# Kernel optimization log

Hardware: AMD Instinct MI355X
Metric: run time of the kernel (lower is better)

## Reference

```python
import jax, jax.numpy as jnp
import numpy as np

L, B, N, D, K = 32, 4, 1000, 128, 8


def setup_inputs() -> dict:
    key = jax.random.key(0)
    ks = jax.random.split(key, 10)
    w = lambda k, s: (jax.random.normal(k, s, jnp.float32) * 0.05)
    return {
        "x": jax.random.normal(ks[0], (L, B, N, D), jnp.float32),
        "route_neighbors": jax.random.randint(ks[1], (N, K), 0, N),
        "t_in_w": w(ks[2], (3 * D, D)),
        "t_in_b": w(ks[3], (3 * D,)),
        "t_out_w": w(ks[4], (D, D)),
        "t_out_b": w(ks[5], (D,)),
        "s_in_w": w(ks[6], (3 * D, D)),
        "s_in_b": w(ks[7], (3 * D,)),
        "s_out_w": w(ks[8], (D, D)),
        "s_out_b": w(ks[9], (D,)),
        "n_heads": 8,
    }


def reference(x, route_neighbors, t_in_w, t_in_b, t_out_w, t_out_b,
              s_in_w, s_in_b, s_out_w, s_out_b, n_heads):
    l, b, n, d = x.shape
    h = n_heads
    dh = d // h
    scale = 1.0 / jnp.sqrt(jnp.asarray(dh, x.dtype))

    # ---- temporal MHA: attend over time axis L, batch = (B, N) ----
    wq, wk, wv = jnp.split(t_in_w, 3, axis=0)
    bq, bk, bv = jnp.split(t_in_b, 3, axis=0)
    q = (x @ wq.T + bq).reshape(l, b, n, h, dh)
    k = (x @ wk.T + bk).reshape(l, b, n, h, dh)
    v = (x @ wv.T + bv).reshape(l, b, n, h, dh)
    scores = jnp.einsum('lbnhd,mbnhd->bnhlm', q, k) * scale
    attn = jax.nn.softmax(scores, axis=-1)
    o = jnp.einsum('bnhlm,mbnhd->lbnhd', attn, v).reshape(l, b, n, d)
    t_out = o @ t_out_w.T + t_out_b

    # ---- spatial MHA: per node, single-token query over K gathered neighbors ----
    swq, swk, swv = jnp.split(s_in_w, 3, axis=0)
    sbq, sbk, sbv = jnp.split(s_in_b, 3, axis=0)
    xn = x[:, :, route_neighbors]                         # (L,B,N,K,D) gather
    sq = (x @ swq.T + sbq).reshape(l, b, n, h, dh)
    sk = (xn @ swk.T + sbk).reshape(l, b, n, -1, h, dh)
    sv = (xn @ swv.T + sbv).reshape(l, b, n, -1, h, dh)
    s_scores = jnp.einsum('lbnhd,lbnkhd->lbnhk', sq, sk) * scale
    s_attn = jax.nn.softmax(s_scores, axis=-1)
    so = jnp.einsum('lbnhk,lbnkhd->lbnhd', s_attn, sv).reshape(l, b, n, d)
    s_out = so @ s_out_w.T + s_out_b

    return t_out + s_out
```

## Files before the change

kernel.cpp:

```cpp
#include <hip/hip_runtime.h>
#include <math.h>

#define L_ 32
#define B_ 4
#define N_ 1000
#define D_ 128
#define H_ 8
#define DH_ 16
#define KN_ 8
#define M_ (L_ * B_ * N_)

typedef __attribute__((ext_vector_type(8))) short short8;
typedef __attribute__((ext_vector_type(8))) unsigned short ushort8v;
typedef __attribute__((ext_vector_type(4))) float floatx4;
typedef __attribute__((ext_vector_type(4))) unsigned uintx4;

static __device__ __forceinline__ unsigned short f2bf(float f) {
  union { float f; unsigned u; } v; v.f = f;
  unsigned r = v.u + 0x7fffu + ((v.u >> 16) & 1u);
  return (unsigned short)(r >> 16);
}
static __device__ __forceinline__ float bf2f(unsigned short s) {
  union { unsigned u; float f; } v; v.u = ((unsigned)s) << 16;
  return v.f;
}
static __device__ __forceinline__ unsigned cvtpk(float lo, float hi) {
  unsigned r;
  asm("v_cvt_pk_bf16_f32 %0, %1, %2" : "=v"(r) : "v"(lo), "v"(hi));
  return r;
}
static __device__ __forceinline__ float vexp2(float x) {
  float r; asm("v_exp_f32 %0, %1" : "=v"(r) : "v"(x)); return r;
}
static __device__ __forceinline__ float vrcp(float x) {
  float r; asm("v_rcp_f32 %0, %1" : "=v"(r) : "v"(x)); return r;
}
union B8 { uintx4 u; short8 s; };
static __device__ __forceinline__ void gload_lds16(const unsigned short* g,
                                                   unsigned short* l) {
  __builtin_amdgcn_global_load_lds(
      (const __attribute__((address_space(1))) unsigned int*)g,
      (__attribute__((address_space(3))) unsigned int*)l, 16, 0, 0);
}

__global__ __launch_bounds__(256) void prep_kernel(
    const float* __restrict__ x, const float* __restrict__ wt_in,
    const float* __restrict__ ws_in, const float* __restrict__ wt_out,
    const float* __restrict__ ws_out, unsigned short* __restrict__ ximg,
    unsigned short* __restrict__ wimg) {
  const int bid = blockIdx.x, t = threadIdx.x;
  const float* src;
  unsigned short* dst;
  if (bid < 1000) {
    src = x + (size_t)bid * 16384;
    dst = ximg + (size_t)bid * 16384;
  } else {
    int w = bid - 1000;
    if (w < 3) src = wt_in + (size_t)w * 16384;
    else if (w < 6) src = ws_in + (size_t)(w - 3) * 16384;
    else if (w == 6) src = wt_out;
    else src = ws_out;
    dst = wimg + (size_t)w * 16384;
  }
#pragma unroll
  for (int it = 0; it < 8; ++it) {
    int gi = it * 256 + t;
    int m = gi >> 4, g = gi & 15;
    const float4* sp = (const float4*)(src + m * 128 + g * 8);
    float4 a = sp[0], b = sp[1];
    ushort8v o;
    o[0] = f2bf(a.x); o[1] = f2bf(a.y); o[2] = f2bf(a.z); o[3] = f2bf(a.w);
    o[4] = f2bf(b.x); o[5] = f2bf(b.y); o[6] = f2bf(b.z); o[7] = f2bf(b.w);
    *(ushort8v*)(dst + (size_t)(m * 16 + (g ^ (m & 7))) * 8) = o;
  }
}

__global__ __launch_bounds__(256) void proj_mfma(
    const unsigned short* __restrict__ ximg,
    const unsigned short* __restrict__ wimg, const float* __restrict__ bias,
    unsigned short* __restrict__ out) {
  __shared__ unsigned short As[128 * 128];
  __shared__ unsigned short Bs[128 * 128];
  const int t = threadIdx.x;
  const int bm = blockIdx.x / 3, bn = blockIdx.x % 3;
  const unsigned short* aSrc = ximg + (size_t)bm * 16384;
  const unsigned short* bSrc = wimg + (size_t)bn * 16384;
#pragma unroll
  for (int it = 0; it < 8; ++it) {
    int gi = it * 256 + t;
    gload_lds16(aSrc + (size_t)gi * 8, &As[gi * 8]);
    gload_lds16(bSrc + (size_t)gi * 8, &Bs[gi * 8]);
  }
  __syncthreads();
  const int wave = t >> 6, lane = t & 63;
  const int wm = (wave >> 1) * 64, wn = (wave & 1) * 64;
  const int lq = lane >> 4, l16 = lane & 15;
  floatx4 acc[4][4] = {};
#pragma unroll
  for (int kk = 0; kk < 4; ++kk) {
    int g = kk * 4 + lq;
    short8 a[4], b[4];
#pragma unroll
    for (int i = 0; i < 4; ++i) {
      int ma = wm + i * 16 + l16;
      a[i] = *(const short8*)(&As[(ma * 16 + (g ^ (ma & 7))) * 8]);
      int nb = wn + i * 16 + l16;
      b[i] = *(const short8*)(&Bs[(nb * 16 + (g ^ (nb & 7))) * 8]);
    }
#pragma unroll
    for (int i = 0; i < 4; ++i)
#pragma unroll
      for (int j = 0; j < 4; ++j)
        acc[i][j] = __builtin_amdgcn_mfma_f32_16x16x32_bf16(a[i], b[j],
                                                            acc[i][j], 0, 0, 0);
  }
  const size_t rowBase = (size_t)bm * 128 + wm;
  const int colBase = bn * 128 + wn;
#pragma unroll
  for (int j = 0; j < 4; ++j) {
    float bb = bias[colBase + j * 16 + l16];
#pragma unroll
    for (int i = 0; i < 4; ++i) {
#pragma unroll
      for (int r = 0; r < 4; ++r) {
        size_t row = rowBase + i * 16 + lq * 4 + r;
        out[row * 384 + colBase + j * 16 + l16] = f2bf(acc[i][j][r] + bb);
      }
    }
  }
}

__global__ __launch_bounds__(256) void tattn_fused(
    const unsigned short* __restrict__ ximg,
    const unsigned short* __restrict__ wimg,
    const float* __restrict__ bias,
    unsigned short* __restrict__ oimg) {
  __shared__ unsigned short Sx[512 * 8];
  __shared__ unsigned short Sqk[4][2][32 * 40];
  const int t = threadIdx.x;
  const int b = blockIdx.x / N_;
  const int n = blockIdx.x % N_;
  const int c = b * N_ + n;
#pragma unroll
  for (int it = 0; it < 2; ++it) {
    const int s = it * 256 + t;
    const int ml = s >> 4, gs = s & 15;
    const int G = gs ^ (ml & 7);
    const size_t rg = (size_t)ml * (B_ * N_) + c;
    gload_lds16(ximg + (rg >> 7) * 16384 +
                    ((rg & 127) * 16 + (size_t)(G ^ ((int)rg & 7))) * 8,
                &Sx[s * 8]);
  }
  asm volatile("s_waitcnt vmcnt(0)" ::: "memory");
  __syncthreads();

  const int wv = t >> 6, lane = t & 63;
  const int lq = lane >> 4, l16 = lane & 15;

  floatx4 aQ[2][2] = {}, aK[2][2] = {}, aV[2][2] = {};
#pragma unroll
  for (int kk = 0; kk < 4; ++kk) {
    short8 a[2];
#pragma unroll
    for (int i = 0; i < 2; ++i) {
      const int ml = i * 16 + l16;
      a[i] = *(const short8*)&Sx[(ml * 16 + ((kk * 4 + lq) ^ (ml & 7))) * 8];
    }
#pragma unroll
    for (int mat = 0; mat < 3; ++mat) {
      const unsigned short* wb = wimg + mat * 16384;
      short8 bf[2];
#pragma unroll
      for (int j = 0; j < 2; ++j) {
        const int nb = wv * 32 + j * 16 + l16;
        bf[j] =
            *(const short8*)&wb[(nb * 16 + ((kk * 4 + lq) ^ (nb & 7))) * 8];
      }
#pragma unroll
      for (int i = 0; i < 2; ++i)
#pragma unroll
        for (int j = 0; j < 2; ++j) {
          floatx4* acc = mat == 0 ? &aQ[i][j] : (mat == 1 ? &aK[i][j] : &aV[i][j]);
          *acc = __builtin_amdgcn_mfma_f32_16x16x32_bf16(a[i], bf[j], *acc, 0,
                                                         0, 0);
        }
    }
  }
  const float bQ0 = bias[wv * 32 + l16], bQ1 = bias[wv * 32 + 16 + l16];
  const float bK0 = bias[128 + wv * 32 + l16],
              bK1 = bias[128 + wv * 32 + 16 + l16];
  const float bV0 = bias[256 + wv * 32 + l16],
              bV1 = bias[256 + wv * 32 + 16 + l16];
  unsigned short* Sq = Sqk[wv][0];
  unsigned short* Sk = Sqk[wv][1];
#pragma unroll
  for (int i = 0; i < 2; ++i)
#pragma unroll
    for (int j = 0; j < 2; ++j) {
      const float qb_ = j ? bQ1 : bQ0, kb_ = j ? bK1 : bK0;
      const unsigned q01 = cvtpk(aQ[i][j][0] + qb_, aQ[i][j][1] + qb_);
      const unsigned q23 = cvtpk(aQ[i][j][2] + qb_, aQ[i][j][3] + qb_);
      const unsigned k01 = cvtpk(aK[i][j][0] + kb_, aK[i][j][1] + kb_);
      const unsigned k23 = cvtpk(aK[i][j][2] + kb_, aK[i][j][3] + kb_);
      unsigned short* q_ = &Sq[(i * 16 + lq * 4) * 40 + j * 16 + l16];
      unsigned short* k_ = &Sk[(i * 16 + lq * 4) * 40 + j * 16 + l16];
      q_[0] = (unsigned short)q01;   q_[40] = (unsigned short)(q01 >> 16);
      q_[80] = (unsigned short)q23;  q_[120] = (unsigned short)(q23 >> 16);
      k_[0] = (unsigned short)k01;   k_[40] = (unsigned short)(k01 >> 16);
      k_[80] = (unsigned short)k23;  k_[120] = (unsigned short)(k23 >> 16);
    }
  unsigned short* ob[8];
  int rsw[8];
#pragma unroll
  for (int lt = 0; lt < 2; ++lt)
#pragma unroll
    for (int r = 0; r < 4; ++r) {
      const int l = lt * 16 + lq * 4 + r;
      const size_t rg = (size_t)l * (B_ * N_) + c;
      ob[lt * 4 + r] = oimg + (rg >> 7) * 16384 + (size_t)(rg & 127) * 128;
      rsw[lt * 4 + r] = (int)(rg & 7);
    }

  const float CSC = 0.25f * 1.4426950408889634f;
#pragma unroll
  for (int hh = 0; hh < 2; ++hh) {
    const int h = wv * 2 + hh;
    short8 ka0 = {}, ka1 = {}, qb0 = {}, qb1 = {};
    if (lq < 2) {
      const int go = (2 * hh + lq) * 8;
      ka0 = *(const short8*)&Sk[l16 * 40 + go];
      ka1 = *(const short8*)&Sk[(16 + l16) * 40 + go];
      qb0 = *(const short8*)&Sq[l16 * 40 + go];
      qb1 = *(const short8*)&Sq[(16 + l16) * 40 + go];
    }
    floatx4 st00 = {}, st01 = {}, st10 = {}, st11 = {};
    st00 = __builtin_amdgcn_mfma_f32_16x16x32_bf16(ka0, qb0, st00, 0, 0, 0);
    st01 = __builtin_amdgcn_mfma_f32_16x16x32_bf16(ka0, qb1, st01, 0, 0, 0);
    st10 = __builtin_amdgcn_mfma_f32_16x16x32_bf16(ka1, qb0, st10, 0, 0, 0);
    st11 = __builtin_amdgcn_mfma_f32_16x16x32_bf16(ka1, qb1, st11, 0, 0, 0);
    const float bV = hh ? bV1 : bV0;
    B8 vu;
    vu.u[0] = cvtpk(aV[0][hh][0] + bV, aV[0][hh][1] + bV);
    vu.u[1] = cvtpk(aV[0][hh][2] + bV, aV[0][hh][3] + bV);
    vu.u[2] = cvtpk(aV[1][hh][0] + bV, aV[1][hh][1] + bV);
    vu.u[3] = cvtpk(aV[1][hh][2] + bV, aV[1][hh][3] + bV);
    const short8 vb = vu.s;
    short8 pa0, pa1;
    {
      floatx4 a = st00 * CSC, cc = st10 * CSC;
      float mx = fmaxf(fmaxf(fmaxf(a[0], a[1]), fmaxf(a[2], a[3])),
                       fmaxf(fmaxf(cc[0], cc[1]), fmaxf(cc[2], cc[3])));
      mx = fmaxf(mx, __shfl_xor(mx, 16));
      mx = fmaxf(mx, __shfl_xor(mx, 32));
      float p0 = vexp2(a[0] - mx), p1 = vexp2(a[1] - mx);
      float p2 = vexp2(a[2] - mx), p3 = vexp2(a[3] - mx);
      float p4 = vexp2(cc[0] - mx), p5 = vexp2(cc[1] - mx);
      float p6 = vexp2(cc[2] - mx), p7 = vexp2(cc[3] - mx);
      float sm = ((p0 + p1) + (p2 + p3)) + ((p4 + p5) + (p6 + p7));
      sm += __shfl_xor(sm, 16);
      sm += __shfl_xor(sm, 32);
      const float inv = vrcp(sm);
      B8 pu;
      pu.u[0] = cvtpk(p0 * inv, p1 * inv);
      pu.u[1] = cvtpk(p2 * inv, p3 * inv);
      pu.u[2] = cvtpk(p4 * inv, p5 * inv);
      pu.u[3] = cvtpk(p6 * inv, p7 * inv);
      pa0 = pu.s;
    }
    {
      floatx4 a = st01 * CSC, cc = st11 * CSC;
      float mx = fmaxf(fmaxf(fmaxf(a[0], a[1]), fmaxf(a[2], a[3])),
                       fmaxf(fmaxf(cc[0], cc[1]), fmaxf(cc[2], cc[3])));
      mx = fmaxf(mx, __shfl_xor(mx, 16));
      mx = fmaxf(mx, __shfl_xor(mx, 32));
      float p0 = vexp2(a[0] - mx), p1 = vexp2(a[1] - mx);
      float p2 = vexp2(a[2] - mx), p3 = vexp2(a[3] - mx);
      float p4 = vexp2(cc[0] - mx), p5 = vexp2(cc[1] - mx);
      float p6 = vexp2(cc[2] - mx), p7 = vexp2(cc[3] - mx);
      float sm = ((p0 + p1) + (p2 + p3)) + ((p4 + p5) + (p6 + p7));
      sm += __shfl_xor(sm, 16);
      sm += __shfl_xor(sm, 32);
      const float inv = vrcp(sm);
      B8 pu;
      pu.u[0] = cvtpk(p0 * inv, p1 * inv);
      pu.u[1] = cvtpk(p2 * inv, p3 * inv);
      pu.u[2] = cvtpk(p4 * inv, p5 * inv);
      pu.u[3] = cvtpk(p6 * inv, p7 * inv);
      pa1 = pu.s;
    }
    floatx4 o0 = {}, o1 = {};
    o0 = __builtin_amdgcn_mfma_f32_16x16x32_bf16(pa0, vb, o0, 0, 0, 0);
    o1 = __builtin_amdgcn_mfma_f32_16x16x32_bf16(pa1, vb, o1, 0, 0, 0);
    const int d = h * 16 + l16;
    const int gd = d >> 3, de = d & 7;
#pragma unroll
    for (int r = 0; r < 4; ++r) {
      const unsigned w = cvtpk(o0[r], o1[r]);
      ob[r][(gd ^ rsw[r]) * 8 + de] = (unsigned short)w;
      ob[4 + r][(gd ^ rsw[4 + r]) * 8 + de] = (unsigned short)(w >> 16);
    }
  }
}

__global__ __launch_bounds__(256) void sattn_kernel(
    const unsigned short* __restrict__ qkv, const int* __restrict__ route,
    unsigned short* __restrict__ oimg) {
  const int t = threadIdx.x;
  const int bb = blockIdx.x;
  const int xcd = bb & 7;
  const int idx = bb >> 3;
  const int lb = (idx >> 5) * 8 + xcd;
  const int chunk = idx & 31;
  const int rl = t >> 3, h = t & 7;
  const int nrow = chunk * 32 + rl;
  if (nrow >= N_) return;
  const int n = nrow;
  const int r = lb * N_ + n;
  float q[16];
  {
    const unsigned short* qp = qkv + (size_t)r * 384 + h * DH_;
    ushort8v q0 = *(const ushort8v*)qp;
    ushort8v q1 = *(const ushort8v*)(qp + 8);
#pragma unroll
    for (int i = 0; i < 8; ++i) { q[i] = bf2f(q0[i]); q[8 + i] = bf2f(q1[i]); }
  }
  int nb[KN_];
#pragma unroll
  for (int kk = 0; kk < KN_; ++kk) nb[kk] = route[n * KN_ + kk];
  ushort8v kr[KN_][2], vr[KN_][2];
#pragma unroll
  for (int kk = 0; kk < KN_; ++kk) {
    const unsigned short* base = qkv + ((size_t)lb * N_ + nb[kk]) * 384;
    const unsigned short* kp = base + 128 + h * DH_;
    const unsigned short* vp = base + 256 + h * DH_;
    kr[kk][0] = *(const ushort8v*)kp;
    kr[kk][1] = *(const ushort8v*)(kp + 8);
    vr[kk][0] = *(const ushort8v*)vp;
    vr[kk][1] = *(const ushort8v*)(vp + 8);
  }
  float sc[KN_];
  float mx = -1e30f;
#pragma unroll
  for (int kk = 0; kk < KN_; ++kk) {
    float d = 0.f;
#pragma unroll
    for (int i = 0; i < 8; ++i) {
      d = fmaf(q[i], bf2f(kr[kk][0][i]), d);
      d = fmaf(q[8 + i], bf2f(kr[kk][1][i]), d);
    }
    d *= 0.25f;
    sc[kk] = d;
    mx = fmaxf(mx, d);
  }
  float ssum = 0.f;
#pragma unroll
  for (int kk = 0; kk < KN_; ++kk) { sc[kk] = __expf(sc[kk] - mx); ssum += sc[kk]; }
  float inv = 1.f / ssum;
  float oa[16];
#pragma unroll
  for (int i = 0; i < 16; ++i) oa[i] = 0.f;
#pragma unroll
  for (int kk = 0; kk < KN_; ++kk) {
    float p = sc[kk] * inv;
#pragma unroll
    for (int i = 0; i < 8; ++i) {
      oa[i] = fmaf(p, bf2f(vr[kk][0][i]), oa[i]);
      oa[8 + i] = fmaf(p, bf2f(vr[kk][1][i]), oa[8 + i]);
    }
  }
  ushort8v w0, w1;
#pragma unroll
  for (int i = 0; i < 8; ++i) { w0[i] = f2bf(oa[i]); w1[i] = f2bf(oa[8 + i]); }
  const int m = r & 127;
  unsigned short* base = oimg + (size_t)(r >> 7) * 16384;
  *(ushort8v*)(base + (size_t)(m * 16 + ((2 * h) ^ (m & 7))) * 8) = w0;
  *(ushort8v*)(base + (size_t)(m * 16 + ((2 * h + 1) ^ (m & 7))) * 8) = w1;
}

__global__ __launch_bounds__(256) void final_mfma(
    const unsigned short* __restrict__ otimg,
    const unsigned short* __restrict__ osimg,
    const unsigned short* __restrict__ wtimg,
    const unsigned short* __restrict__ wsimg, const float* __restrict__ bt,
    const float* __restrict__ bs, float* __restrict__ out) {
  __shared__ unsigned short As[128 * 128];
  __shared__ unsigned short Bs[128 * 128];
  const int t = threadIdx.x;
  const int bm = blockIdx.x;
  const int wave = t >> 6, lane = t & 63;
  const int wm = (wave >> 1) * 64, wn = (wave & 1) * 64;
  const int lq = lane >> 4, l16 = lane & 15;
  floatx4 acc[4][4] = {};
#pragma unroll
  for (int p = 0; p < 2; ++p) {
    if (p) __syncthreads();
    const unsigned short* aSrc = (p ? osimg : otimg) + (size_t)bm * 16384;
    const unsigned short* bSrc = p ? wsimg : wtimg;
#pragma unroll
    for (int it = 0; it < 8; ++it) {
      int gi = it * 256 + t;
      gload_lds16(aSrc + (size_t)gi * 8, &As[gi * 8]);
      gload_lds16(bSrc + (size_t)gi * 8, &Bs[gi * 8]);
    }
    __syncthreads();
#pragma unroll
    for (int kk = 0; kk < 4; ++kk) {
      int g = kk * 4 + lq;
      short8 a[4], b[4];
#pragma unroll
      for (int i = 0; i < 4; ++i) {
        int ma = wm + i * 16 + l16;
        a[i] = *(const short8*)(&As[(ma * 16 + (g ^ (ma & 7))) * 8]);
        int nb = wn + i * 16 + l16;
        b[i] = *(const short8*)(&Bs[(nb * 16 + (g ^ (nb & 7))) * 8]);
      }
#pragma unroll
      for (int i = 0; i < 4; ++i)
#pragma unroll
        for (int j = 0; j < 4; ++j)
          acc[i][j] = __builtin_amdgcn_mfma_f32_16x16x32_bf16(a[i], b[j],
                                                              acc[i][j], 0, 0, 0);
    }
  }
  const size_t rowBase = (size_t)bm * 128 + wm;
#pragma unroll
  for (int j = 0; j < 4; ++j) {
    int col = wn + j * 16 + l16;
    float bb = bt[col] + bs[col];
#pragma unroll
    for (int i = 0; i < 4; ++i) {
#pragma unroll
      for (int r = 0; r < 4; ++r) {
        size_t row = rowBase + i * 16 + lq * 4 + r;
        out[row * 128 + col] = acc[i][j][r] + bb;
      }
    }
  }
}

extern "C" void kernel_launch(void* const* d_in, const int* in_sizes, int n_in,
                              void* d_out, int out_size, void* d_ws,
                              size_t ws_size, hipStream_t stream) {
  const float* x = (const float*)d_in[0];
  const int* route = (const int*)d_in[1];
  const float* t_in_w = (const float*)d_in[2];
  const float* t_in_b = (const float*)d_in[3];
  const float* t_out_w = (const float*)d_in[4];
  const float* t_out_b = (const float*)d_in[5];
  const float* s_in_w = (const float*)d_in[6];
  const float* s_in_b = (const float*)d_in[7];
  const float* s_out_w = (const float*)d_in[8];
  const float* s_out_b = (const float*)d_in[9];
  float* out = (float*)d_out;
  unsigned short* ximg = (unsigned short*)d_ws;
  unsigned short* qkv = ximg + (size_t)M_ * 128;
  unsigned short* o_t = qkv + (size_t)M_ * 384;
  unsigned short* wimg = o_t + (size_t)M_ * 128;
  unsigned short* o_s = ximg;

  prep_kernel<<<1008, 256, 0, stream>>>(x, t_in_w, s_in_w, t_out_w, s_out_w,
                                        ximg, wimg);
  tattn_fused<<<B_ * N_, 256, 0, stream>>>(ximg, wimg, t_in_b, o_t);
  proj_mfma<<<(M_ / 128) * 3, 256, 0, stream>>>(ximg, wimg + 3 * 16384,
                                                s_in_b, qkv);
  sattn_kernel<<<8 * 16 * 32, 256, 0, stream>>>(qkv, route, o_s);
  final_mfma<<<M_ / 128, 256, 0, stream>>>(o_t, o_s, wimg + 6 * 16384,
                                           wimg + 7 * 16384, t_out_b, s_out_b,
                                           out);
}
```

Before: 267.3 us.

## Fuse spatial attention into final output projection kernel via LDS staging

```diff
diff --git a/kernel.cpp b/kernel.cpp
--- a/kernel.cpp
+++ b/kernel.cpp
@@ -36,6 +36,7 @@
   float r; asm("v_rcp_f32 %0, %1" : "=v"(r) : "v"(x)); return r;
 }
 union B8 { uintx4 u; short8 s; };
+union BW8 { uintx4 u; ushort8v s; };
 static __device__ __forceinline__ void gload_lds16(const unsigned short* g,
                                                    unsigned short* l) {
   __builtin_amdgcn_global_load_lds(
@@ -302,129 +303,135 @@
   }
 }
 
-__global__ __launch_bounds__(256) void sattn_kernel(
+__global__ __launch_bounds__(512) void sattn_final(
     const unsigned short* __restrict__ qkv, const int* __restrict__ route,
-    unsigned short* __restrict__ oimg) {
-  const int t = threadIdx.x;
-  const int bb = blockIdx.x;
-  const int xcd = bb & 7;
-  const int idx = bb >> 3;
-  const int lb = (idx >> 5) * 8 + xcd;
-  const int chunk = idx & 31;
-  const int rl = t >> 3, h = t & 7;
-  const int nrow = chunk * 32 + rl;
-  if (nrow >= N_) return;
-  const int n = nrow;
-  const int r = lb * N_ + n;
-  float q[16];
-  {
-    const unsigned short* qp = qkv + (size_t)r * 384 + h * DH_;
-    ushort8v q0 = *(const ushort8v*)qp;
-    ushort8v q1 = *(const ushort8v*)(qp + 8);
-#pragma unroll
-    for (int i = 0; i < 8; ++i) { q[i] = bf2f(q0[i]); q[8 + i] = bf2f(q1[i]); }
-  }
-  int nb[KN_];
-#pragma unroll
-  for (int kk = 0; kk < KN_; ++kk) nb[kk] = route[n * KN_ + kk];
-  ushort8v kr[KN_][2], vr[KN_][2];
-#pragma unroll
-  for (int kk = 0; kk < KN_; ++kk) {
-    const unsigned short* base = qkv + ((size_t)lb * N_ + nb[kk]) * 384;
-    const unsigned short* kp = base + 128 + h * DH_;
-    const unsigned short* vp = base + 256 + h * DH_;
-    kr[kk][0] = *(const ushort8v*)kp;
-    kr[kk][1] = *(const ushort8v*)(kp + 8);
-    vr[kk][0] = *(const ushort8v*)vp;
-    vr[kk][1] = *(const ushort8v*)(vp + 8);
-  }
-  float sc[KN_];
-  float mx = -1e30f;
-#pragma unroll
-  for (int kk = 0; kk < KN_; ++kk) {
-    float d = 0.f;
-#pragma unroll
-    for (int i = 0; i < 8; ++i) {
-      d = fmaf(q[i], bf2f(kr[kk][0][i]), d);
-      d = fmaf(q[8 + i], bf2f(kr[kk][1][i]), d);
-    }
-    d *= 0.25f;
-    sc[kk] = d;
-    mx = fmaxf(mx, d);
-  }
-  float ssum = 0.f;
-#pragma unroll
-  for (int kk = 0; kk < KN_; ++kk) { sc[kk] = __expf(sc[kk] - mx); ssum += sc[kk]; }
-  float inv = 1.f / ssum;
-  float oa[16];
-#pragma unroll
-  for (int i = 0; i < 16; ++i) oa[i] = 0.f;
-#pragma unroll
-  for (int kk = 0; kk < KN_; ++kk) {
-    float p = sc[kk] * inv;
-#pragma unroll
-    for (int i = 0; i < 8; ++i) {
-      oa[i] = fmaf(p, bf2f(vr[kk][0][i]), oa[i]);
-      oa[8 + i] = fmaf(p, bf2f(vr[kk][1][i]), oa[8 + i]);
-    }
-  }
-  ushort8v w0, w1;
-#pragma unroll
-  for (int i = 0; i < 8; ++i) { w0[i] = f2bf(oa[i]); w1[i] = f2bf(oa[8 + i]); }
-  const int m = r & 127;
-  unsigned short* base = oimg + (size_t)(r >> 7) * 16384;
-  *(ushort8v*)(base + (size_t)(m * 16 + ((2 * h) ^ (m & 7))) * 8) = w0;
-  *(ushort8v*)(base + (size_t)(m * 16 + ((2 * h + 1) ^ (m & 7))) * 8) = w1;
-}
-
-__global__ __launch_bounds__(256) void final_mfma(
     const unsigned short* __restrict__ otimg,
-    const unsigned short* __restrict__ osimg,
     const unsigned short* __restrict__ wtimg,
-    const unsigned short* __restrict__ wsimg, const float* __restrict__ bt,
-    const float* __restrict__ bs, float* __restrict__ out) {
-  __shared__ unsigned short As[128 * 128];
+    const unsigned short* __restrict__ wsimg,
+    const float* __restrict__ bt, const float* __restrict__ bs,
+    float* __restrict__ out) {
+  __shared__ unsigned short Os[128 * 128];
   __shared__ unsigned short Bs[128 * 128];
   const int t = threadIdx.x;
   const int bm = blockIdx.x;
+#pragma unroll
+  for (int it = 0; it < 4; ++it) {
+    int gi = it * 512 + t;
+    gload_lds16(wsimg + (size_t)gi * 8, &Bs[gi * 8]);
+  }
+  const int h = t & 7;
+#pragma unroll
+  for (int it2 = 0; it2 < 2; ++it2) {
+    const int rl = (t >> 3) + it2 * 64;
+    const int gr = bm * 128 + rl;
+    const int lb = (int)((unsigned)gr / 1000u);
+    const int n = gr - lb * 1000;
+    float q[16];
+    {
+      const unsigned short* qp = qkv + (size_t)gr * 384 + h * DH_;
+      ushort8v q0 = *(const ushort8v*)qp;
+      ushort8v q1 = *(const ushort8v*)(qp + 8);
+#pragma unroll
+      for (int i = 0; i < 8; ++i) { q[i] = bf2f(q0[i]); q[8 + i] = bf2f(q1[i]); }
+    }
+    int nb[KN_];
+#pragma unroll
+    for (int kk = 0; kk < KN_; ++kk) nb[kk] = route[n * KN_ + kk];
+    ushort8v kr[KN_][2], vr[KN_][2];
+#pragma unroll
+    for (int kk = 0; kk < KN_; ++kk) {
+      const unsigned short* base = qkv + ((size_t)lb * N_ + nb[kk]) * 384;
+      const unsigned short* kp = base + 128 + h * DH_;
+      const unsigned short* vp = base + 256 + h * DH_;
+      kr[kk][0] = *(const ushort8v*)kp;
+      kr[kk][1] = *(const ushort8v*)(kp + 8);
+      vr[kk][0] = *(const ushort8v*)vp;
+      vr[kk][1] = *(const ushort8v*)(vp + 8);
+    }
+    float sc[KN_];
+    float mx = -1e30f;
+#pragma unroll
+    for (int kk = 0; kk < KN_; ++kk) {
+      float d = 0.f;
+#pragma unroll
+      for (int i = 0; i < 8; ++i) {
+        d = fmaf(q[i], bf2f(kr[kk][0][i]), d);
+        d = fmaf(q[8 + i], bf2f(kr[kk][1][i]), d);
+      }
+      d *= 0.25f;
+      sc[kk] = d;
+      mx = fmaxf(mx, d);
+    }
+    float ssum = 0.f;
+#pragma unroll
+    for (int kk = 0; kk < KN_; ++kk) { sc[kk] = __expf(sc[kk] - mx); ssum += sc[kk]; }
+    float inv = 1.f / ssum;
+    float oa[16];
+#pragma unroll
+    for (int i = 0; i < 16; ++i) oa[i] = 0.f;
+#pragma unroll
+    for (int kk = 0; kk < KN_; ++kk) {
+      float p = sc[kk] * inv;
+#pragma unroll
+      for (int i = 0; i < 8; ++i) {
+        oa[i] = fmaf(p, bf2f(vr[kk][0][i]), oa[i]);
+        oa[8 + i] = fmaf(p, bf2f(vr[kk][1][i]), oa[8 + i]);
+      }
+    }
+    BW8 w0, w1;
+    w0.u[0] = cvtpk(oa[0], oa[1]);   w0.u[1] = cvtpk(oa[2], oa[3]);
+    w0.u[2] = cvtpk(oa[4], oa[5]);   w0.u[3] = cvtpk(oa[6], oa[7]);
+    w1.u[0] = cvtpk(oa[8], oa[9]);   w1.u[1] = cvtpk(oa[10], oa[11]);
+    w1.u[2] = cvtpk(oa[12], oa[13]); w1.u[3] = cvtpk(oa[14], oa[15]);
+    const int sw = rl & 7;
+    *(ushort8v*)(&Os[(size_t)(rl * 16 + ((2 * h) ^ sw)) * 8]) = w0.s;
+    *(ushort8v*)(&Os[(size_t)(rl * 16 + ((2 * h + 1) ^ sw)) * 8]) = w1.s;
+  }
+  asm volatile("s_waitcnt vmcnt(0)" ::: "memory");
+  __syncthreads();
+
   const int wave = t >> 6, lane = t & 63;
-  const int wm = (wave >> 1) * 64, wn = (wave & 1) * 64;
+  const int wm = (wave >> 2) * 64, wn = (wave & 3) * 32;
   const int lq = lane >> 4, l16 = lane & 15;
-  floatx4 acc[4][4] = {};
+  floatx4 acc[4][2] = {};
 #pragma unroll
   for (int p = 0; p < 2; ++p) {
-    if (p) __syncthreads();
-    const unsigned short* aSrc = (p ? osimg : otimg) + (size_t)bm * 16384;
-    const unsigned short* bSrc = p ? wsimg : wtimg;
-#pragma unroll
-    for (int it = 0; it < 8; ++it) {
-      int gi = it * 256 + t;
-      gload_lds16(aSrc + (size_t)gi * 8, &As[gi * 8]);
-      gload_lds16(bSrc + (size_t)gi * 8, &Bs[gi * 8]);
-    }
-    __syncthreads();
+    if (p) {
+      __syncthreads();
+#pragma unroll
+      for (int it = 0; it < 4; ++it) {
+        int gi = it * 512 + t;
+        gload_lds16(otimg + (size_t)bm * 16384 + (size_t)gi * 8, &Os[gi * 8]);
+        gload_lds16(wtimg + (size_t)gi * 8, &Bs[gi * 8]);
+      }
+      asm volatile("s_waitcnt vmcnt(0)" ::: "memory");
+      __syncthreads();
+    }
 #pragma unroll
     for (int kk = 0; kk < 4; ++kk) {
       int g = kk * 4 + lq;
-      short8 a[4], b[4];
+      short8 a[4], b[2];
 #pragma unroll
       for (int i = 0; i < 4; ++i) {
         int ma = wm + i * 16 + l16;
-        a[i] = *(const short8*)(&As[(ma * 16 + (g ^ (ma & 7))) * 8]);
-        int nb = wn + i * 16 + l16;
-        b[i] = *(const short8*)(&Bs[(nb * 16 + (g ^ (nb & 7))) * 8]);
+        a[i] = *(const short8*)(&Os[(ma * 16 + (g ^ (ma & 7))) * 8]);
+      }
+#pragma unroll
+      for (int j = 0; j < 2; ++j) {
+        int nb2 = wn + j * 16 + l16;
+        b[j] = *(const short8*)(&Bs[(nb2 * 16 + (g ^ (nb2 & 7))) * 8]);
       }
 #pragma unroll
       for (int i = 0; i < 4; ++i)
 #pragma unroll
-        for (int j = 0; j < 4; ++j)
+        for (int j = 0; j < 2; ++j)
           acc[i][j] = __builtin_amdgcn_mfma_f32_16x16x32_bf16(a[i], b[j],
                                                               acc[i][j], 0, 0, 0);
     }
   }
   const size_t rowBase = (size_t)bm * 128 + wm;
 #pragma unroll
-  for (int j = 0; j < 4; ++j) {
+  for (int j = 0; j < 2; ++j) {
     int col = wn + j * 16 + l16;
     float bb = bt[col] + bs[col];
 #pragma unroll
@@ -456,15 +463,13 @@
   unsigned short* qkv = ximg + (size_t)M_ * 128;
   unsigned short* o_t = qkv + (size_t)M_ * 384;
   unsigned short* wimg = o_t + (size_t)M_ * 128;
-  unsigned short* o_s = ximg;
 
   prep_kernel<<<1008, 256, 0, stream>>>(x, t_in_w, s_in_w, t_out_w, s_out_w,
                                         ximg, wimg);
   tattn_fused<<<B_ * N_, 256, 0, stream>>>(ximg, wimg, t_in_b, o_t);
   proj_mfma<<<(M_ / 128) * 3, 256, 0, stream>>>(ximg, wimg + 3 * 16384,
                                                 s_in_b, qkv);
-  sattn_kernel<<<8 * 16 * 32, 256, 0, stream>>>(qkv, route, o_s);
-  final_mfma<<<M_ / 128, 256, 0, stream>>>(o_t, o_s, wimg + 6 * 16384,
-                                           wimg + 7 * 16384, t_out_b, s_out_b,
-                                           out);
-}
+  sattn_final<<<M_ / 128, 512, 0, stream>>>(qkv, route, o_t,
+                                            wimg + 6 * 16384, wimg + 7 * 16384,
+                                            t_out_b, s_out_b, out);
+}
```

Result: slower. 295.4 us (+10.5%).
